# Kernel tuning notes

Measured on AMD Instinct MI355X. Metric: run time of the kernel, lower is better.

Reference implementation:

```python
import jax, jax.numpy as jnp
import numpy as np

H = 1024          # h_dim
FF = 4 * H
E = 8             # num_expert
TOP_K = 2


def setup_inputs() -> dict:
    key = jax.random.key(0)
    ks = jax.random.split(key, 7)
    B, S = 4, 2048
    s = 0.02
    return {
        "x": jax.random.normal(ks[0], (B, S, H), dtype=jnp.float32),
        "Wg": jax.random.normal(ks[1], (H, E), dtype=jnp.float32) * s,
        "bg": jnp.zeros((E,), dtype=jnp.float32),
        "W1": jax.random.normal(ks[2], (E, H, FF), dtype=jnp.float32) * s,
        "b1": jnp.zeros((E, FF), dtype=jnp.float32),
        "W2": jax.random.normal(ks[3], (E, FF, H), dtype=jnp.float32) * s,
        "b2": jnp.zeros((E, H), dtype=jnp.float32),
    }


def _moe(x, Wg, bg, W1, b1, W2, b2):
    B, S, h = x.shape
    hs = x.reshape(-1, h)                                  # [T, H]
    logits = hs @ Wg + bg                                  # [T, E]
    probs = jax.nn.softmax(logits.astype(jnp.float32), axis=-1)
    w, idx = jax.lax.top_k(probs, TOP_K)                   # [T, K]
    w = jax.nn.softmax(w, axis=-1).astype(x.dtype)         # renormalize over top-k
    out = jnp.zeros_like(hs)
    for e in range(E):
        # per-token combine weight for expert e (0 if not selected)
        w_e = jnp.sum(w * (idx == e), axis=-1)             # [T]
        y = jax.nn.relu(hs @ W1[e] + b1[e]) @ W2[e] + b2[e]  # [T, H]
        out = out + w_e[:, None] * y
    return out.reshape(B, S, h), logits


def reference(x, Wg, bg, W1, b1, W2, b2):
    return _moe(x, Wg, bg, W1, b1, W2, b2)
```

## Files before the change

### kernel.cpp

```cpp
#include <hip/hip_runtime.h>
#include <hip/hip_bf16.h>

#define T_TOKENS 8192
#define HD 1024
#define FF 4096
#define NEXP 8
#define NR_MAX 17408

typedef __attribute__((ext_vector_type(8))) short bf16x8;
typedef __attribute__((ext_vector_type(4))) float f32x4;
typedef unsigned short ushort8v __attribute__((ext_vector_type(8)));

static __device__ __forceinline__ float b2f(ushort u) {
    union { unsigned u; float f; } c; c.u = ((unsigned)u) << 16; return c.f;
}
static __device__ __forceinline__ ushort f2b(float f) {
    union { float f; unsigned u; } c; c.f = f;
    unsigned r = c.u + 0x7fffu + ((c.u >> 16) & 1u);
    return (ushort)(r >> 16);
}

__global__ __launch_bounds__(256) void gate_kernel(
    const float* __restrict__ x, const float* __restrict__ Wg, const float* __restrict__ bg,
    float* __restrict__ logits, int* __restrict__ counts,
    int* __restrict__ e0a, int* __restrict__ e1a,
    float* __restrict__ w0a, float* __restrict__ w1a)
{
    int t = blockIdx.x * 4 + (threadIdx.x >> 6);
    int l = threadIdx.x & 63;
    const float* xr = x + (size_t)t * HD;
    float acc[8] = {0,0,0,0,0,0,0,0};
    #pragma unroll
    for (int i = 0; i < 4; ++i) {
        int h0 = i * 256 + l * 4;
        float4 xv = *(const float4*)(xr + h0);
        #pragma unroll
        for (int j = 0; j < 4; ++j) {
            float xs = (&xv.x)[j];
            const float4* wr = (const float4*)(Wg + (size_t)(h0 + j) * NEXP);
            float4 wa = wr[0], wb = wr[1];
            acc[0] = fmaf(xs, wa.x, acc[0]);
            acc[1] = fmaf(xs, wa.y, acc[1]);
            acc[2] = fmaf(xs, wa.z, acc[2]);
            acc[3] = fmaf(xs, wa.w, acc[3]);
            acc[4] = fmaf(xs, wb.x, acc[4]);
            acc[5] = fmaf(xs, wb.y, acc[5]);
            acc[6] = fmaf(xs, wb.z, acc[6]);
            acc[7] = fmaf(xs, wb.w, acc[7]);
        }
    }
    #pragma unroll
    for (int off = 32; off > 0; off >>= 1) {
        #pragma unroll
        for (int e = 0; e < 8; ++e) acc[e] += __shfl_down(acc[e], off, 64);
    }
    if (l == 0) {
        float lg[8];
        #pragma unroll
        for (int e = 0; e < 8; ++e) {
            lg[e] = acc[e] + bg[e];
            logits[(size_t)t * NEXP + e] = lg[e];
        }
        float m = lg[0];
        #pragma unroll
        for (int e = 1; e < 8; ++e) m = fmaxf(m, lg[e]);
        float p[8], s = 0.f;
        #pragma unroll
        for (int e = 0; e < 8; ++e) { p[e] = expf(lg[e] - m); s += p[e]; }
        float inv = 1.f / s;
        #pragma unroll
        for (int e = 0; e < 8; ++e) p[e] *= inv;
        int i0 = 0;
        #pragma unroll
        for (int e = 1; e < 8; ++e) if (p[e] > p[i0]) i0 = e;
        int i1 = (i0 == 0) ? 1 : 0;
        #pragma unroll
        for (int e = 0; e < 8; ++e) if (e != i0 && p[e] > p[i1]) i1 = e;
        float ed = expf(p[i1] - p[i0]);
        float w0 = 1.f / (1.f + ed);
        float w1 = ed / (1.f + ed);
        e0a[t] = i0; e1a[t] = i1; w0a[t] = w0; w1a[t] = w1;
        atomicAdd(&counts[i0], 1);
        atomicAdd(&counts[i1], 1);
    }
}

__global__ __launch_bounds__(256) void assign_kernel(
    const int* __restrict__ e0a, const int* __restrict__ e1a,
    const int* __restrict__ counts, int* __restrict__ fill, int* __restrict__ offg,
    int* __restrict__ row0, int* __restrict__ row1, int* __restrict__ row_token)
{
    __shared__ int off[9];
    if (threadIdx.x == 0) {
        int o = 0;
        #pragma unroll
        for (int e = 0; e < 8; ++e) { off[e] = o; o += (counts[e] + 127) & ~127; }
        off[8] = o;
        if (blockIdx.x == 0) {
            #pragma unroll
            for (int i = 0; i < 9; ++i) offg[i] = off[i];
        }
    }
    __syncthreads();
    int t = blockIdx.x * 256 + threadIdx.x;
    if (t >= T_TOKENS) return;
    int e0 = e0a[t];
    int r0 = off[e0] + atomicAdd(&fill[e0], 1);
    row0[t] = r0; row_token[r0] = t;
    int e1 = e1a[t];
    int r1 = off[e1] + atomicAdd(&fill[e1], 1);
    row1[t] = r1; row_token[r1] = t;
}

__global__ __launch_bounds__(256) void gather_kernel(
    const float* __restrict__ x, const int* __restrict__ row_token, ushort* __restrict__ Xp)
{
    int r = blockIdx.x * 2 + (threadIdx.x >> 7);
    int c = (threadIdx.x & 127) * 8;
    int tok = row_token[r];
    ushort8v o;
    if (tok >= 0 && tok < T_TOKENS) {
        const float* src = x + (size_t)tok * HD + c;
        float4 v1 = *(const float4*)(src);
        float4 v2 = *(const float4*)(src + 4);
        o[0] = f2b(v1.x); o[1] = f2b(v1.y); o[2] = f2b(v1.z); o[3] = f2b(v1.w);
        o[4] = f2b(v2.x); o[5] = f2b(v2.y); o[6] = f2b(v2.z); o[7] = f2b(v2.w);
    } else {
        o = (ushort8v){0,0,0,0,0,0,0,0};
    }
    *(ushort8v*)(Xp + (size_t)r * HD + c) = o;
}

__global__ __launch_bounds__(256) void transpose_cvt_all(
    const float* __restrict__ W1, const float* __restrict__ W2,
    ushort* __restrict__ W1T, ushort* __restrict__ W2T)
{
    __shared__ float tile[64][65];
    int b = blockIdx.x;
    const float* in; ushort* out; int R, C, tid2, clog;
    if (b < 8192) {
        int e = b >> 10; tid2 = b & 1023;
        in = W1 + (size_t)e * HD * FF; out = W1T + (size_t)e * HD * FF;
        R = HD; C = FF; clog = 6;
    } else {
        int bb = b - 8192; int e = bb >> 10; tid2 = bb & 1023;
        in = W2 + (size_t)e * FF * HD; out = W2T + (size_t)e * FF * HD;
        R = FF; C = HD; clog = 4;
    }
    int rt = tid2 >> clog, ct = tid2 & ((1 << clog) - 1);
    int r0 = rt * 64, c0 = ct * 64;

    int tr = threadIdx.x >> 4;
    int tc = (threadIdx.x & 15) * 4;
    #pragma unroll
    for (int i = 0; i < 4; ++i) {
        int r = tr + i * 16;
        float4 v = *(const float4*)(in + (size_t)(r0 + r) * C + c0 + tc);
        tile[r][tc + 0] = v.x;
        tile[r][tc + 1] = v.y;
        tile[r][tc + 2] = v.z;
        tile[r][tc + 3] = v.w;
    }
    __syncthreads();
    int cc = threadIdx.x >> 3;
    int rr = (threadIdx.x & 7) * 8;
    #pragma unroll
    for (int i = 0; i < 2; ++i) {
        int c = cc + i * 32;
        ushort8v o;
        #pragma unroll
        for (int j = 0; j < 8; ++j) o[j] = f2b(tile[rr + j][c]);
        *(ushort8v*)(out + (size_t)(c0 + c) * R + r0 + rr) = o;
    }
}

template<int K, int NTOT, bool RELU, bool MFAST>
__global__ __launch_bounds__(256, 4) void gemm_kernel(
    const ushort* __restrict__ A, const ushort* __restrict__ Bt,
    const float* __restrict__ bias, ushort* __restrict__ Out,
    const int* __restrict__ off)
{
    constexpr int NT = NTOT / 128;
    __shared__ __align__(16) ushort lds[2][2][128 * 32];

    int nwg = gridDim.x;
    int chunkc = nwg >> 3;
    int cid = blockIdx.x & 7, q = blockIdx.x >> 3;
    int mtile, ntile;
    if constexpr (MFAST) {
        int mloc = chunkc / NT;
        mtile = cid * mloc + q % mloc;
        ntile = q / mloc;
    } else {
        int wgid = cid * chunkc + q;
        ntile = wgid % NT;
        mtile = wgid / NT;
    }
    int r0 = mtile * 128;
    int total = off[8];
    if (r0 >= total) return;
    int e = 0;
    #pragma unroll
    for (int qq = 0; qq < 7; ++qq) if (r0 >= off[qq + 1]) e = qq + 1;

    int tid = threadIdx.x;
    int w = tid >> 6, lane = tid & 63;
    int wr = w >> 1, wc = w & 1;
    int lr = lane & 15, lk = lane >> 4;

    const ushort* Ab = A + (size_t)r0 * K;
    const ushort* Bb = Bt + ((size_t)e * NTOT + (size_t)ntile * 128) * K;

    auto stage = [&](const ushort* gbase, ushort* ldsbase) {
        #pragma unroll
        for (int issue = 0; issue < 2; ++issue) {
            int row = issue * 64 + w * 16 + (lane >> 2);
            int chunk = (lane & 3) ^ ((lane >> 3) & 3);
            const ushort* g = gbase + (size_t)row * K + chunk * 8;
            ushort* lp = ldsbase + (issue * 64 + w * 16) * 32;
            __builtin_amdgcn_global_load_lds(
                (const __attribute__((address_space(1))) void*)g,
                (__attribute__((address_space(3))) void*)lp, 16, 0, 0);
        }
    };

    stage(Ab, &lds[0][0][0]);
    stage(Bb, &lds[0][1][0]);

    f32x4 acc[4][4];
    #pragma unroll
    for (int mi = 0; mi < 4; ++mi)
        #pragma unroll
        for (int ni = 0; ni < 4; ++ni) acc[mi][ni] = (f32x4){0.f, 0.f, 0.f, 0.f};

    __syncthreads();

    constexpr int KT = K / 32;
    int cur = 0;
    int slot = lk ^ ((lr >> 1) & 3);
    for (int kt = 0; kt < KT; ++kt) {
        if (kt + 1 < KT) {
            stage(Ab + (kt + 1) * 32, &lds[cur ^ 1][0][0]);
            stage(Bb + (kt + 1) * 32, &lds[cur ^ 1][1][0]);
        }
        const ushort* As = &lds[cur][0][0];
        const ushort* Bs = &lds[cur][1][0];
        bf16x8 a[4], b[4];
        #pragma unroll
        for (int mi = 0; mi < 4; ++mi)
            a[mi] = *(const bf16x8*)(As + (wr * 64 + mi * 16 + lr) * 32 + slot * 8);
        #pragma unroll
        for (int ni = 0; ni < 4; ++ni)
            b[ni] = *(const bf16x8*)(Bs + (wc * 64 + ni * 16 + lr) * 32 + slot * 8);
        #pragma unroll
        for (int mi = 0; mi < 4; ++mi)
            #pragma unroll
            for (int ni = 0; ni < 4; ++ni)
                acc[mi][ni] = __builtin_amdgcn_mfma_f32_16x16x32_bf16(
                    a[mi], b[ni], acc[mi][ni], 0, 0, 0);
        __syncthreads();
        cur ^= 1;
    }

    int c0 = ntile * 128 + wc * 64;
    int rbase = r0 + wr * 64;
    #pragma unroll
    for (int ni = 0; ni < 4; ++ni) {
        int n = c0 + ni * 16 + lr;
        float bv = bias[(size_t)e * NTOT + n];
        #pragma unroll
        for (int mi = 0; mi < 4; ++mi) {
            int m = rbase + mi * 16 + lk * 4;
            #pragma unroll
            for (int j = 0; j < 4; ++j) {
                float v = acc[mi][ni][j] + bv;
                if (RELU) v = fmaxf(v, 0.f);
                Out[(size_t)(m + j) * NTOT + n] = f2b(v);
            }
        }
    }
}

__global__ __launch_bounds__(256) void combine_kernel(
    const ushort* __restrict__ Y, const int* __restrict__ row0, const int* __restrict__ row1,
    const float* __restrict__ w0a, const float* __restrict__ w1a, float* __restrict__ out)
{
    int t = blockIdx.x;
    int c = threadIdx.x * 4;
    int r0 = row0[t], r1 = row1[t];
    float w0 = w0a[t], w1 = w1a[t];
    ushort4 ya = *(const ushort4*)(Y + (size_t)r0 * HD + c);
    ushort4 yb = *(const ushort4*)(Y + (size_t)r1 * HD + c);
    float4 o;
    o.x = w0 * b2f(ya.x) + w1 * b2f(yb.x);
    o.y = w0 * b2f(ya.y) + w1 * b2f(yb.y);
    o.z = w0 * b2f(ya.z) + w1 * b2f(yb.z);
    o.w = w0 * b2f(ya.w) + w1 * b2f(yb.w);
    *(float4*)(out + (size_t)t * HD + c) = o;
}

#define WSA(x) (((x) + 255) & ~(size_t)255)
static constexpr size_t OFF_COUNTS = 0;
static constexpr size_t OFF_FILL   = 64;
static constexpr size_t OFF_OFF    = 128;
static constexpr size_t OFF_E0     = 256;
static constexpr size_t OFF_E1     = OFF_E0 + (size_t)T_TOKENS * 4;
static constexpr size_t OFF_W0     = OFF_E1 + (size_t)T_TOKENS * 4;
static constexpr size_t OFF_W1A    = OFF_W0 + (size_t)T_TOKENS * 4;
static constexpr size_t OFF_R0     = OFF_W1A + (size_t)T_TOKENS * 4;
static constexpr size_t OFF_R1     = OFF_R0 + (size_t)T_TOKENS * 4;
static constexpr size_t OFF_RT     = OFF_R1 + (size_t)T_TOKENS * 4;
static constexpr size_t OFF_XP     = WSA(OFF_RT + (size_t)NR_MAX * 4);
static constexpr size_t OFF_W1T    = OFF_XP  + (size_t)NR_MAX * HD * 2;
static constexpr size_t OFF_W2T    = OFF_W1T + (size_t)NEXP * FF * HD * 2;
static constexpr size_t OFF_H1     = OFF_W2T + (size_t)NEXP * HD * FF * 2;
static constexpr size_t OFF_Y      = OFF_H1  + (size_t)NR_MAX * FF * 2;
static constexpr size_t WS_NEEDED  = OFF_Y   + (size_t)NR_MAX * HD * 2;

extern "C" void kernel_launch(void* const* d_in, const int* in_sizes, int n_in,
                              void* d_out, int out_size, void* d_ws, size_t ws_size,
                              hipStream_t stream) {
    (void)in_sizes; (void)n_in; (void)out_size;
    const float* x  = (const float*)d_in[0];
    const float* Wg = (const float*)d_in[1];
    const float* bg = (const float*)d_in[2];
    const float* W1 = (const float*)d_in[3];
    const float* b1 = (const float*)d_in[4];
    const float* W2 = (const float*)d_in[5];
    const float* b2 = (const float*)d_in[6];
    float* out    = (float*)d_out;
    float* logits = out + (size_t)T_TOKENS * HD;

    if (ws_size < WS_NEEDED) return;

    char* ws = (char*)d_ws;
    int*    counts = (int*)(ws + OFF_COUNTS);
    int*    fill   = (int*)(ws + OFF_FILL);
    int*    offp   = (int*)(ws + OFF_OFF);
    int*    e0a    = (int*)(ws + OFF_E0);
    int*    e1a    = (int*)(ws + OFF_E1);
    float*  w0a    = (float*)(ws + OFF_W0);
    float*  w1a    = (float*)(ws + OFF_W1A);
    int*    row0   = (int*)(ws + OFF_R0);
    int*    row1   = (int*)(ws + OFF_R1);
    int*    rowtok = (int*)(ws + OFF_RT);
    ushort* Xp     = (ushort*)(ws + OFF_XP);
    ushort* W1T    = (ushort*)(ws + OFF_W1T);
    ushort* W2T    = (ushort*)(ws + OFF_W2T);
    ushort* H1     = (ushort*)(ws + OFF_H1);
    ushort* Y      = (ushort*)(ws + OFF_Y);

    hipMemsetAsync(ws, 0, 256, stream);
    hipMemsetAsync(rowtok, 0xFF, (size_t)NR_MAX * 4, stream);

    gate_kernel<<<T_TOKENS / 4, 256, 0, stream>>>(x, Wg, bg, logits, counts, e0a, e1a, w0a, w1a);
    assign_kernel<<<T_TOKENS / 256, 256, 0, stream>>>(e0a, e1a, counts, fill, offp, row0, row1, rowtok);
    gather_kernel<<<NR_MAX / 2, 256, 0, stream>>>(x, rowtok, Xp);
    transpose_cvt_all<<<8192 + 8192, 256, 0, stream>>>(W1, W2, W1T, W2T);
    gemm_kernel<HD, FF, true, true>
        <<<(FF / 128) * (NR_MAX / 128), 256, 0, stream>>>(Xp, W1T, b1, H1, offp);
    gemm_kernel<FF, HD, false, false>
        <<<(HD / 128) * (NR_MAX / 128), 256, 0, stream>>>(H1, W2T, b2, Y, offp);
    combine_kernel<<<T_TOKENS, 256, 0, stream>>>(Y, row0, row1, w0a, w1a, out);
}
```

Baseline: 772.5 us.

## Add triple-buffered 128x256 direct-to-LDS GEMM for second expert projection

Adds a new grouped GEMM kernel for the down projection (FF to H). It uses a 128x256 tile, triple-buffered LDS filled by global_load_lds with an XOR swizzle, split-phase MFMA with explicit waitcnt and barriers, setprio, and an XCD-aware workgroup remap. Only the second GEMM moves to it. The goal is to hide global load latency and raise MFMA utilisation, at the cost of more registers and LDS per block and fragile hand-written synchronisation.

```diff
diff --git a/kernel.cpp b/kernel.cpp
--- a/kernel.cpp
+++ b/kernel.cpp
@@ -266,6 +266,149 @@
     int rbase = r0 + wr * 64;
     #pragma unroll
     for (int ni = 0; ni < 4; ++ni) {
+        int n = c0 + ni * 16 + lr;
+        float bv = bias[(size_t)e * NTOT + n];
+        #pragma unroll
+        for (int mi = 0; mi < 4; ++mi) {
+            int m = rbase + mi * 16 + lk * 4;
+            #pragma unroll
+            for (int j = 0; j < 4; ++j) {
+                float v = acc[mi][ni][j] + bv;
+                if (RELU) v = fmaxf(v, 0.f);
+                Out[(size_t)(m + j) * NTOT + n] = f2b(v);
+            }
+        }
+    }
+}
+
+template<int K, int NTOT, bool RELU>
+__global__ __launch_bounds__(256, 2) void gemm_ph_kernel(
+    const ushort* __restrict__ A, const ushort* __restrict__ Bt,
+    const float* __restrict__ bias, ushort* __restrict__ Out,
+    const int* __restrict__ off)
+{
+    constexpr int BM = 128, BN = 256, BK = 32;
+    constexpr int KT = K / BK;
+    constexpr int NT = NTOT / BN;
+    __shared__ __align__(16) ushort Al[3][BM * BK];
+    __shared__ __align__(16) ushort Bl[3][BN * BK];
+
+    int nwg = gridDim.x;
+    int wgid = (blockIdx.x & 7) * (nwg >> 3) + (blockIdx.x >> 3);
+    int ntile = wgid % NT;
+    int mtile = wgid / NT;
+    int r0 = mtile * BM;
+    int total = off[8];
+    if (r0 >= total) return;
+    int e = 0;
+    #pragma unroll
+    for (int qq = 0; qq < 7; ++qq) if (r0 >= off[qq + 1]) e = qq + 1;
+
+    int tid = threadIdx.x;
+    int wid = tid >> 6, lane = tid & 63;
+    int wr = wid >> 1, wc = wid & 1;
+    int lr = lane & 15, lk = lane >> 4;
+
+    const ushort* Ab = A + (size_t)r0 * K;
+    const ushort* Bb = Bt + ((size_t)e * NTOT + (size_t)ntile * BN) * K;
+
+    auto stageA = [&](int kt, int sl) {
+        #pragma unroll
+        for (int i = 0; i < 2; ++i) {
+            int sidx = i * 256 + tid;
+            int row = sidx >> 2, ch = sidx & 3;
+            int sch = ch ^ ((row >> 1) & 3);
+            const ushort* g = Ab + (size_t)row * K + kt * 32 + sch * 8;
+            __builtin_amdgcn_global_load_lds(
+                (const __attribute__((address_space(1))) void*)g,
+                (__attribute__((address_space(3))) void*)(&Al[sl][0] + sidx * 8), 16, 0, 0);
+        }
+    };
+    auto stageB = [&](int kt, int sl) {
+        #pragma unroll
+        for (int i = 0; i < 4; ++i) {
+            int sidx = i * 256 + tid;
+            int row = sidx >> 2, ch = sidx & 3;
+            int sch = ch ^ ((row >> 1) & 3);
+            const ushort* g = Bb + (size_t)row * K + kt * 32 + sch * 8;
+            __builtin_amdgcn_global_load_lds(
+                (const __attribute__((address_space(1))) void*)g,
+                (__attribute__((address_space(3))) void*)(&Bl[sl][0] + sidx * 8), 16, 0, 0);
+        }
+    };
+    int rchunk = lk ^ ((lr >> 1) & 3);
+    auto ldA = [&](int sl, int mi) -> bf16x8 {
+        int row = wr * 64 + mi * 16 + lr;
+        return *(const bf16x8*)&Al[sl][row * 32 + rchunk * 8];
+    };
+    auto ldB = [&](int sl, int ni) -> bf16x8 {
+        int row = wc * 128 + ni * 16 + lr;
+        return *(const bf16x8*)&Bl[sl][row * 32 + rchunk * 8];
+    };
+
+    f32x4 acc[4][8];
+    #pragma unroll
+    for (int mi = 0; mi < 4; ++mi)
+        #pragma unroll
+        for (int ni = 0; ni < 8; ++ni) acc[mi][ni] = (f32x4){0.f, 0.f, 0.f, 0.f};
+
+    stageA(0, 0); stageB(0, 0);
+    stageA(1, 1); stageB(1, 1);
+    asm volatile("s_waitcnt vmcnt(6)" ::: "memory");
+    __builtin_amdgcn_sched_barrier(0);
+    __builtin_amdgcn_s_barrier();
+
+    int sl = 0, sn = 2;
+    for (int kt = 0; kt < KT; ++kt) {
+        int kc = (kt + 2 < KT) ? (kt + 2) : (KT - 1);
+        bf16x8 a[4], b[4];
+        #pragma unroll
+        for (int mi = 0; mi < 4; ++mi) a[mi] = ldA(sl, mi);
+        #pragma unroll
+        for (int ni = 0; ni < 4; ++ni) b[ni] = ldB(sl, ni);
+        stageA(kc, sn);
+        __builtin_amdgcn_s_barrier();
+        asm volatile("s_waitcnt lgkmcnt(0)" ::: "memory");
+        __builtin_amdgcn_sched_barrier(0);
+        __builtin_amdgcn_s_setprio(1);
+        #pragma unroll
+        for (int mi = 0; mi < 4; ++mi)
+            #pragma unroll
+            for (int ni = 0; ni < 4; ++ni)
+                acc[mi][ni] = __builtin_amdgcn_mfma_f32_16x16x32_bf16(
+                    a[mi], b[ni], acc[mi][ni], 0, 0, 0);
+        __builtin_amdgcn_sched_barrier(0);
+        __builtin_amdgcn_s_setprio(0);
+        __builtin_amdgcn_s_barrier();
+
+        #pragma unroll
+        for (int ni = 0; ni < 4; ++ni) b[ni] = ldB(sl, 4 + ni);
+        stageB(kc, sn);
+        __builtin_amdgcn_s_barrier();
+        asm volatile("s_waitcnt lgkmcnt(0)" ::: "memory");
+        __builtin_amdgcn_sched_barrier(0);
+        __builtin_amdgcn_s_setprio(1);
+        #pragma unroll
+        for (int mi = 0; mi < 4; ++mi)
+            #pragma unroll
+            for (int ni = 0; ni < 4; ++ni)
+                acc[mi][4 + ni] = __builtin_amdgcn_mfma_f32_16x16x32_bf16(
+                    a[mi], b[ni], acc[mi][4 + ni], 0, 0, 0);
+        __builtin_amdgcn_sched_barrier(0);
+        __builtin_amdgcn_s_setprio(0);
+        asm volatile("s_waitcnt vmcnt(6)" ::: "memory");
+        __builtin_amdgcn_sched_barrier(0);
+        __builtin_amdgcn_s_barrier();
+
+        sl = (sl == 2) ? 0 : sl + 1;
+        sn = (sn == 2) ? 0 : sn + 1;
+    }
+    asm volatile("s_waitcnt vmcnt(0)" ::: "memory");
+
+    int c0 = ntile * BN + wc * 128;
+    int rbase = r0 + wr * 64;
+    #pragma unroll
+    for (int ni = 0; ni < 8; ++ni) {
         int n = c0 + ni * 16 + lr;
         float bv = bias[(size_t)e * NTOT + n];
         #pragma unroll
@@ -359,7 +502,7 @@
     transpose_cvt_all<<<8192 + 8192, 256, 0, stream>>>(W1, W2, W1T, W2T);
     gemm_kernel<HD, FF, true, true>
         <<<(FF / 128) * (NR_MAX / 128), 256, 0, stream>>>(Xp, W1T, b1, H1, offp);
-    gemm_kernel<FF, HD, false, false>
-        <<<(HD / 128) * (NR_MAX / 128), 256, 0, stream>>>(H1, W2T, b2, Y, offp);
+    gemm_ph_kernel<FF, HD, false>
+        <<<(HD / 256) * (NR_MAX / 128), 256, 0, stream>>>(H1, W2T, b2, Y, offp);
     combine_kernel<<<T_TOKENS, 256, 0, stream>>>(Y, row0, row1, w0a, w1a, out);
 }
```

Result: slower. 807.8 us (+4.6%).

## Overlap weight transposes with gate and first expert GEMM via fused launches

Applied to the files above, without the earlier changes.

Splits the combined W1/W2 transpose-convert kernel into two parts. The W1 transpose now runs as extra blocks of the gate kernel, and the W2 transpose runs as extra blocks of a specialized first-GEMM kernel. The aim is to fill idle compute units during the small gate kernel and the partially filled GEMM1, hiding the memory-bound transpose work and saving a launch. The cost is code duplication and heavier per-block branching, and the transpose blocks may contend with GEMM blocks for bandwidth and occupancy.

```diff
diff --git a/kernel.cpp b/kernel.cpp
--- a/kernel.cpp
+++ b/kernel.cpp
@@ -20,68 +20,103 @@
     return (ushort)(r >> 16);
 }
 
-__global__ __launch_bounds__(256) void gate_kernel(
+__global__ __launch_bounds__(256) void gate_w1t_kernel(
     const float* __restrict__ x, const float* __restrict__ Wg, const float* __restrict__ bg,
     float* __restrict__ logits, int* __restrict__ counts,
     int* __restrict__ e0a, int* __restrict__ e1a,
-    float* __restrict__ w0a, float* __restrict__ w1a)
-{
-    int t = blockIdx.x * 4 + (threadIdx.x >> 6);
-    int l = threadIdx.x & 63;
-    const float* xr = x + (size_t)t * HD;
-    float acc[8] = {0,0,0,0,0,0,0,0};
-    #pragma unroll
-    for (int i = 0; i < 4; ++i) {
-        int h0 = i * 256 + l * 4;
-        float4 xv = *(const float4*)(xr + h0);
-        #pragma unroll
-        for (int j = 0; j < 4; ++j) {
-            float xs = (&xv.x)[j];
-            const float4* wr = (const float4*)(Wg + (size_t)(h0 + j) * NEXP);
-            float4 wa = wr[0], wb = wr[1];
-            acc[0] = fmaf(xs, wa.x, acc[0]);
-            acc[1] = fmaf(xs, wa.y, acc[1]);
-            acc[2] = fmaf(xs, wa.z, acc[2]);
-            acc[3] = fmaf(xs, wa.w, acc[3]);
-            acc[4] = fmaf(xs, wb.x, acc[4]);
-            acc[5] = fmaf(xs, wb.y, acc[5]);
-            acc[6] = fmaf(xs, wb.z, acc[6]);
-            acc[7] = fmaf(xs, wb.w, acc[7]);
-        }
-    }
-    #pragma unroll
-    for (int off = 32; off > 0; off >>= 1) {
-        #pragma unroll
-        for (int e = 0; e < 8; ++e) acc[e] += __shfl_down(acc[e], off, 64);
-    }
-    if (l == 0) {
-        float lg[8];
-        #pragma unroll
-        for (int e = 0; e < 8; ++e) {
-            lg[e] = acc[e] + bg[e];
-            logits[(size_t)t * NEXP + e] = lg[e];
-        }
-        float m = lg[0];
-        #pragma unroll
-        for (int e = 1; e < 8; ++e) m = fmaxf(m, lg[e]);
-        float p[8], s = 0.f;
-        #pragma unroll
-        for (int e = 0; e < 8; ++e) { p[e] = expf(lg[e] - m); s += p[e]; }
-        float inv = 1.f / s;
-        #pragma unroll
-        for (int e = 0; e < 8; ++e) p[e] *= inv;
-        int i0 = 0;
-        #pragma unroll
-        for (int e = 1; e < 8; ++e) if (p[e] > p[i0]) i0 = e;
-        int i1 = (i0 == 0) ? 1 : 0;
-        #pragma unroll
-        for (int e = 0; e < 8; ++e) if (e != i0 && p[e] > p[i1]) i1 = e;
-        float ed = expf(p[i1] - p[i0]);
-        float w0 = 1.f / (1.f + ed);
-        float w1 = ed / (1.f + ed);
-        e0a[t] = i0; e1a[t] = i1; w0a[t] = w0; w1a[t] = w1;
-        atomicAdd(&counts[i0], 1);
-        atomicAdd(&counts[i1], 1);
+    float* __restrict__ w0a, float* __restrict__ w1a,
+    const float* __restrict__ W1, ushort* __restrict__ W1T)
+{
+    __shared__ float tile[64][65];
+    if (blockIdx.x < 2048) {
+        int t = blockIdx.x * 4 + (threadIdx.x >> 6);
+        int l = threadIdx.x & 63;
+        const float* xr = x + (size_t)t * HD;
+        float acc[8] = {0,0,0,0,0,0,0,0};
+        #pragma unroll
+        for (int i = 0; i < 4; ++i) {
+            int h0 = i * 256 + l * 4;
+            float4 xv = *(const float4*)(xr + h0);
+            #pragma unroll
+            for (int j = 0; j < 4; ++j) {
+                float xs = (&xv.x)[j];
+                const float4* wr = (const float4*)(Wg + (size_t)(h0 + j) * NEXP);
+                float4 wa = wr[0], wb = wr[1];
+                acc[0] = fmaf(xs, wa.x, acc[0]);
+                acc[1] = fmaf(xs, wa.y, acc[1]);
+                acc[2] = fmaf(xs, wa.z, acc[2]);
+                acc[3] = fmaf(xs, wa.w, acc[3]);
+                acc[4] = fmaf(xs, wb.x, acc[4]);
+                acc[5] = fmaf(xs, wb.y, acc[5]);
+                acc[6] = fmaf(xs, wb.z, acc[6]);
+                acc[7] = fmaf(xs, wb.w, acc[7]);
+            }
+        }
+        #pragma unroll
+        for (int off = 32; off > 0; off >>= 1) {
+            #pragma unroll
+            for (int e = 0; e < 8; ++e) acc[e] += __shfl_down(acc[e], off, 64);
+        }
+        if (l == 0) {
+            float lg[8];
+            #pragma unroll
+            for (int e = 0; e < 8; ++e) {
+                lg[e] = acc[e] + bg[e];
+                logits[(size_t)t * NEXP + e] = lg[e];
+            }
+            float m = lg[0];
+            #pragma unroll
+            for (int e = 1; e < 8; ++e) m = fmaxf(m, lg[e]);
+            float p[8], s = 0.f;
+            #pragma unroll
+            for (int e = 0; e < 8; ++e) { p[e] = expf(lg[e] - m); s += p[e]; }
+            float inv = 1.f / s;
+            #pragma unroll
+            for (int e = 0; e < 8; ++e) p[e] *= inv;
+            int i0 = 0;
+            #pragma unroll
+            for (int e = 1; e < 8; ++e) if (p[e] > p[i0]) i0 = e;
+            int i1 = (i0 == 0) ? 1 : 0;
+            #pragma unroll
+            for (int e = 0; e < 8; ++e) if (e != i0 && p[e] > p[i1]) i1 = e;
+            float ed = expf(p[i1] - p[i0]);
+            float w0 = 1.f / (1.f + ed);
+            float w1 = ed / (1.f + ed);
+            e0a[t] = i0; e1a[t] = i1; w0a[t] = w0; w1a[t] = w1;
+            atomicAdd(&counts[i0], 1);
+            atomicAdd(&counts[i1], 1);
+        }
+    } else {
+        int bb = blockIdx.x - 2048;
+        int e = bb >> 10, tid2 = bb & 1023;
+        const float* in = W1 + (size_t)e * HD * FF;
+        ushort* out = W1T + (size_t)e * HD * FF;
+        int R = HD, C = FF;
+        int rt = tid2 >> 6, ct = tid2 & 63;
+        int r0 = rt * 64, c0 = ct * 64;
+
+        int tr = threadIdx.x >> 4;
+        int tc = (threadIdx.x & 15) * 4;
+        #pragma unroll
+        for (int i = 0; i < 4; ++i) {
+            int r = tr + i * 16;
+            float4 v = *(const float4*)(in + (size_t)(r0 + r) * C + c0 + tc);
+            tile[r][tc + 0] = v.x;
+            tile[r][tc + 1] = v.y;
+            tile[r][tc + 2] = v.z;
+            tile[r][tc + 3] = v.w;
+        }
+        __syncthreads();
+        int cc = threadIdx.x >> 3;
+        int rr = (threadIdx.x & 7) * 8;
+        #pragma unroll
+        for (int i = 0; i < 2; ++i) {
+            int c = cc + i * 32;
+            ushort8v o;
+            #pragma unroll
+            for (int j = 0; j < 8; ++j) o[j] = f2b(tile[rr + j][c]);
+            *(ushort8v*)(out + (size_t)(c0 + c) * R + r0 + rr) = o;
+        }
     }
 }
 
@@ -131,46 +166,139 @@
     *(ushort8v*)(Xp + (size_t)r * HD + c) = o;
 }
 
-__global__ __launch_bounds__(256) void transpose_cvt_all(
-    const float* __restrict__ W1, const float* __restrict__ W2,
-    ushort* __restrict__ W1T, ushort* __restrict__ W2T)
-{
-    __shared__ float tile[64][65];
-    int b = blockIdx.x;
-    const float* in; ushort* out; int R, C, tid2, clog;
-    if (b < 8192) {
-        int e = b >> 10; tid2 = b & 1023;
-        in = W1 + (size_t)e * HD * FF; out = W1T + (size_t)e * HD * FF;
-        R = HD; C = FF; clog = 6;
+__global__ __launch_bounds__(256, 4) void gemm1_w2t_kernel(
+    const ushort* __restrict__ A, const ushort* __restrict__ Bt,
+    const float* __restrict__ bias, ushort* __restrict__ Out,
+    const int* __restrict__ off,
+    const float* __restrict__ W2, ushort* __restrict__ W2T)
+{
+    constexpr int K = HD, NTOT = FF;
+    constexpr int NT = NTOT / 128;
+    constexpr int NWG = (FF / 128) * (NR_MAX / 128);
+    __shared__ __align__(16) char smem[32768];
+
+    if (blockIdx.x < NWG) {
+        ushort* L = (ushort*)smem;
+        constexpr int chunkc = NWG >> 3;
+        int cid = blockIdx.x & 7, q = blockIdx.x >> 3;
+        constexpr int mloc = chunkc / NT;
+        int mtile = cid * mloc + q % mloc;
+        int ntile = q / mloc;
+        int r0 = mtile * 128;
+        int total = off[8];
+        if (r0 >= total) return;
+        int e = 0;
+        #pragma unroll
+        for (int qq = 0; qq < 7; ++qq) if (r0 >= off[qq + 1]) e = qq + 1;
+
+        int tid = threadIdx.x;
+        int w = tid >> 6, lane = tid & 63;
+        int wr = w >> 1, wc = w & 1;
+        int lr = lane & 15, lk = lane >> 4;
+
+        const ushort* Ab = A + (size_t)r0 * K;
+        const ushort* Bb = Bt + ((size_t)e * NTOT + (size_t)ntile * 128) * K;
+
+        auto stage = [&](const ushort* gbase, ushort* ldsbase) {
+            #pragma unroll
+            for (int issue = 0; issue < 2; ++issue) {
+                int row = issue * 64 + w * 16 + (lane >> 2);
+                int chunk = (lane & 3) ^ ((lane >> 3) & 3);
+                const ushort* g = gbase + (size_t)row * K + chunk * 8;
+                ushort* lp = ldsbase + (issue * 64 + w * 16) * 32;
+                __builtin_amdgcn_global_load_lds(
+                    (const __attribute__((address_space(1))) void*)g,
+                    (__attribute__((address_space(3))) void*)lp, 16, 0, 0);
+            }
+        };
+
+        stage(Ab, L + 0 * 4096);
+        stage(Bb, L + 1 * 4096);
+
+        f32x4 acc[4][4];
+        #pragma unroll
+        for (int mi = 0; mi < 4; ++mi)
+            #pragma unroll
+            for (int ni = 0; ni < 4; ++ni) acc[mi][ni] = (f32x4){0.f, 0.f, 0.f, 0.f};
+
+        __syncthreads();
+
+        constexpr int KT = K / 32;
+        int cur = 0;
+        int slot = lk ^ ((lr >> 1) & 3);
+        for (int kt = 0; kt < KT; ++kt) {
+            if (kt + 1 < KT) {
+                stage(Ab + (kt + 1) * 32, L + ((cur ^ 1) * 2 + 0) * 4096);
+                stage(Bb + (kt + 1) * 32, L + ((cur ^ 1) * 2 + 1) * 4096);
+            }
+            const ushort* As = L + (cur * 2 + 0) * 4096;
+            const ushort* Bs = L + (cur * 2 + 1) * 4096;
+            bf16x8 a[4], b[4];
+            #pragma unroll
+            for (int mi = 0; mi < 4; ++mi)
+                a[mi] = *(const bf16x8*)(As + (wr * 64 + mi * 16 + lr) * 32 + slot * 8);
+            #pragma unroll
+            for (int ni = 0; ni < 4; ++ni)
+                b[ni] = *(const bf16x8*)(Bs + (wc * 64 + ni * 16 + lr) * 32 + slot * 8);
+            #pragma unroll
+            for (int mi = 0; mi < 4; ++mi)
+                #pragma unroll
+                for (int ni = 0; ni < 4; ++ni)
+                    acc[mi][ni] = __builtin_amdgcn_mfma_f32_16x16x32_bf16(
+                        a[mi], b[ni], acc[mi][ni], 0, 0, 0);
+            __syncthreads();
+            cur ^= 1;
+        }
+
+        int c0 = ntile * 128 + wc * 64;
+        int rbase = r0 + wr * 64;
+        #pragma unroll
+        for (int ni = 0; ni < 4; ++ni) {
+            int n = c0 + ni * 16 + lr;
+            float bv = bias[(size_t)e * NTOT + n];
+            #pragma unroll
+            for (int mi = 0; mi < 4; ++mi) {
+                int m = rbase + mi * 16 + lk * 4;
+                #pragma unroll
+                for (int j = 0; j < 4; ++j) {
+                    float v = acc[mi][ni][j] + bv;
+                    v = fmaxf(v, 0.f);
+                    Out[(size_t)(m + j) * NTOT + n] = f2b(v);
+                }
+            }
+        }
     } else {
-        int bb = b - 8192; int e = bb >> 10; tid2 = bb & 1023;
-        in = W2 + (size_t)e * FF * HD; out = W2T + (size_t)e * FF * HD;
-        R = FF; C = HD; clog = 4;
-    }
-    int rt = tid2 >> clog, ct = tid2 & ((1 << clog) - 1);
-    int r0 = rt * 64, c0 = ct * 64;
-
-    int tr = threadIdx.x >> 4;
-    int tc = (threadIdx.x & 15) * 4;
-    #pragma unroll
-    for (int i = 0; i < 4; ++i) {
-        int r = tr + i * 16;
-        float4 v = *(const float4*)(in + (size_t)(r0 + r) * C + c0 + tc);
-        tile[r][tc + 0] = v.x;
-        tile[r][tc + 1] = v.y;
-        tile[r][tc + 2] = v.z;
-        tile[r][tc + 3] = v.w;
-    }
-    __syncthreads();
-    int cc = threadIdx.x >> 3;
-    int rr = (threadIdx.x & 7) * 8;
-    #pragma unroll
-    for (int i = 0; i < 2; ++i) {
-        int c = cc + i * 32;
-        ushort8v o;
-        #pragma unroll
-        for (int j = 0; j < 8; ++j) o[j] = f2b(tile[rr + j][c]);
-        *(ushort8v*)(out + (size_t)(c0 + c) * R + r0 + rr) = o;
+        float (*tile)[65] = (float(*)[65])smem;
+        int bb = blockIdx.x - NWG;
+        int e = bb >> 10, tid2 = bb & 1023;
+        const float* in = W2 + (size_t)e * FF * HD;
+        ushort* out = W2T + (size_t)e * FF * HD;
+        int R = FF, C = HD;
+        int rt = tid2 >> 4, ct = tid2 & 15;
+        int r0 = rt * 64, c0 = ct * 64;
+
+        int tr = threadIdx.x >> 4;
+        int tc = (threadIdx.x & 15) * 4;
+        #pragma unroll
+        for (int i = 0; i < 4; ++i) {
+            int r = tr + i * 16;
+            float4 v = *(const float4*)(in + (size_t)(r0 + r) * C + c0 + tc);
+            tile[r][tc + 0] = v.x;
+            tile[r][tc + 1] = v.y;
+            tile[r][tc + 2] = v.z;
+            tile[r][tc + 3] = v.w;
+        }
+        __syncthreads();
+        int cc = threadIdx.x >> 3;
+        int rr = (threadIdx.x & 7) * 8;
+        #pragma unroll
+        for (int i = 0; i < 2; ++i) {
+            int c = cc + i * 32;
+            ushort8v o;
+            #pragma unroll
+            for (int j = 0; j < 8; ++j) o[j] = f2b(tile[rr + j][c]);
+            *(ushort8v*)(out + (size_t)(c0 + c) * R + r0 + rr) = o;
+        }
     }
 }
 
@@ -353,12 +481,12 @@
     hipMemsetAsync(ws, 0, 256, stream);
     hipMemsetAsync(rowtok, 0xFF, (size_t)NR_MAX * 4, stream);
 
-    gate_kernel<<<T_TOKENS / 4, 256, 0, stream>>>(x, Wg, bg, logits, counts, e0a, e1a, w0a, w1a);
+    gate_w1t_kernel<<<2048 + 8192, 256, 0, stream>>>(
+        x, Wg, bg, logits, counts, e0a, e1a, w0a, w1a, W1, W1T);
     assign_kernel<<<T_TOKENS / 256, 256, 0, stream>>>(e0a, e1a, counts, fill, offp, row0, row1, rowtok);
     gather_kernel<<<NR_MAX / 2, 256, 0, stream>>>(x, rowtok, Xp);
-    transpose_cvt_all<<<8192 + 8192, 256, 0, stream>>>(W1, W2, W1T, W2T);
-    gemm_kernel<HD, FF, true, true>
-        <<<(FF / 128) * (NR_MAX / 128), 256, 0, stream>>>(Xp, W1T, b1, H1, offp);
+    gemm1_w2t_kernel<<<(FF / 128) * (NR_MAX / 128) + 8192, 256, 0, stream>>>(
+        Xp, W1T, b1, H1, offp, W2, W2T);
     gemm_kernel<FF, HD, false, false>
         <<<(HD / 128) * (NR_MAX / 128), 256, 0, stream>>>(H1, W2T, b2, Y, offp);
     combine_kernel<<<T_TOKENS, 256, 0, stream>>>(Y, row0, row1, w0a, w1a, out);
```

After: 734.1 us (median of 2 runs). 5.0% less time.
